# Performance work log

Measured on AMD Instinct MI355X. Metric: run time of the kernel, lower is better.

The kernel has to match this reference:

```python
import jax, jax.numpy as jnp
import numpy as np

B = 131072
D = 64          # d_model
T = 4           # num_tiles
TEMP = 0.5


def setup_inputs() -> dict:
    key = jax.random.key(0)
    ks = jax.random.split(key, 16)
    s = 0.02
    return {
        "a_vec": jax.random.normal(ks[0], (B, D), dtype=jnp.float32),
        "b_vec": jax.random.normal(ks[1], (B, D), dtype=jnp.float32),
        "pos_encoding": jax.random.normal(ks[2], (B, 8), dtype=jnp.float32),
        # router: Linear(2D+8 -> D), GELU, Linear(D -> T)
        "Wr1": jax.random.normal(ks[3], (2 * D + 8, D), dtype=jnp.float32) * s,
        "br1": jnp.zeros((D,), dtype=jnp.float32),
        "Wr2": jax.random.normal(ks[4], (D, T), dtype=jnp.float32) * s,
        "br2": jnp.zeros((T,), dtype=jnp.float32),
        # tile nets: per-tile Linear(2D -> 2D), GELU, Linear(2D -> D)
        "W1": jax.random.normal(ks[5], (T, 2 * D, 2 * D), dtype=jnp.float32) * s,
        "b1": jnp.zeros((T, 2 * D), dtype=jnp.float32),
        "W2": jax.random.normal(ks[6], (T, 2 * D, D), dtype=jnp.float32) * s,
        "b2": jnp.zeros((T, D), dtype=jnp.float32),
    }


def _router(x, Wr1, br1, Wr2, br2):
    h = jax.nn.gelu(x @ Wr1 + br1, approximate=False)  # torch nn.GELU is exact
    return (h @ Wr2 + br2) / TEMP


def reference(a_vec, b_vec, pos_encoding, Wr1, br1, Wr2, br2, W1, b1, W2, b2):
    pair = jnp.concatenate([a_vec, b_vec], axis=-1)            # (B, 2D)

    # Routing 1 uses pair; routing 2 uses flipped pair. Both expert passes
    # consume `pair` (faithful to the original code, which feeds pair both times).
    idx1 = jnp.argmax(_router(jnp.concatenate([pair, pos_encoding], -1),
                              Wr1, br1, Wr2, br2), axis=-1)    # (B,)
    pair_flip = jnp.concatenate([b_vec, a_vec], axis=-1)
    idx2 = jnp.argmax(_router(jnp.concatenate([pair_flip, pos_encoding], -1),
                              Wr1, br1, Wr2, br2), axis=-1)    # (B,)

    # Run all tiles on every sample (small T), then gather the routed output.
    h = jax.nn.gelu(jnp.einsum('bi,tij->btj', pair, W1) + b1, approximate=False)  # (B,T,2D)
    out_all = jnp.einsum('bth,thd->btd', h, W2) + b2                              # (B,T,D)

    out1 = jnp.take_along_axis(out_all, idx1[:, None, None], axis=1)[:, 0]
    out2 = jnp.take_along_axis(out_all, idx2[:, None, None], axis=1)[:, 0]
    return out1, out2
```

## Files before the change

kernel.cpp:

```cpp
#include <hip/hip_runtime.h>

#define B_N 131072

using bfrag_t = __attribute__((ext_vector_type(8))) short;
using acc_t   = __attribute__((ext_vector_type(4))) float;
using v4f     = __attribute__((ext_vector_type(4))) float;
using i32x4_t = __attribute__((ext_vector_type(4))) int;

__device__ __forceinline__ unsigned short f2bf(float f) {
  unsigned int u = __float_as_uint(f);
  u += 0x7FFFu + ((u >> 16) & 1u);
  return (unsigned short)(u >> 16);
}

__device__ __forceinline__ unsigned int pk2bf(float x, float y) {
  return (unsigned int)f2bf(x) | ((unsigned int)f2bf(y) << 16);
}

__device__ __forceinline__ void gload_lds16(const void* g, void* l) {
  __builtin_amdgcn_global_load_lds((const __attribute__((address_space(1))) void*)g,
                                   (__attribute__((address_space(3))) void*)l, 16, 0, 0);
}

__device__ __forceinline__ float gelu_f(float x) {
  float ax = fabsf(x) * 0.70710678118654752f;
  float t  = __builtin_amdgcn_rcpf(fmaf(0.3275911f, ax, 1.0f));
  float p  = fmaf(1.061405429f, t, -1.453152027f);
  p = fmaf(p, t, 1.421413741f);
  p = fmaf(p, t, -0.284496736f);
  p = fmaf(p, t, 0.254829592f);
  p = p * t;
  float e  = __expf(-ax * ax);
  float er = fmaf(-p, e, 1.0f);
  er = (x < 0.0f) ? -er : er;
  return 0.5f * x * (1.0f + er);
}

__global__ __launch_bounds__(256) void prepack2_k(
    const float* __restrict__ Wr1, const float* __restrict__ br1,
    const float* __restrict__ Wr2, const float* __restrict__ br2,
    const float* __restrict__ W1, const float* __restrict__ W2,
    float* __restrict__ RW, short* __restrict__ W1s, short* __restrict__ W2s) {
  int gt = blockIdx.x * 256 + threadIdx.x;
  for (int idx = gt; idx < 142 * 64; idx += 16384) {
    int row = idx >> 6, j = idx & 63; float val;
    if (row < 136)      val = Wr1[row * 64 + j];
    else if (row == 136) val = br1[j];
    else if (row < 141) val = Wr2[(row - 137) * 64 + j];
    else                val = (j < 4) ? br2[j] : 0.0f;
    RW[idx] = val;
  }
  for (int ch = gt; ch < 8192; ch += 16384) {
    int t = ch >> 11, r = (ch >> 4) & 127, c = ch & 15;
    const float* src = W1 + t * 16384 + r;
    short* dst = W1s + (t * 128 + r) * 128 + ((c ^ (r & 15)) * 8);
    #pragma unroll
    for (int m = 0; m < 8; m++) dst[m] = (short)f2bf(src[(c * 8 + m) * 128]);
  }
  for (int ch = gt; ch < 4096; ch += 16384) {
    int t = ch >> 10, d = (ch >> 4) & 63, c = ch & 15;
    const float* src = W2 + t * 8192 + d;
    short* dst = W2s + (t * 64 + d) * 128 + ((c ^ (d & 15)) * 8);
    #pragma unroll
    for (int m = 0; m < 8; m++) dst[m] = (short)f2bf(src[(c * 8 + m) * 64]);
  }
}

__global__ __launch_bounds__(256) void router4_k(
    const float* __restrict__ a, const float* __restrict__ b,
    const float* __restrict__ pos, const float* __restrict__ RW,
    unsigned char* __restrict__ r1, unsigned char* __restrict__ r2) {
  __shared__ float WB[142 * 64];
  int tid = threadIdx.x, wave = tid >> 6, lane = tid & 63;
  for (int it = 0; it < 9; it++) {
    int cb = it * 256 + wave * 64;
    if (cb < 2272) {
      int chunk = cb + lane;
      if (chunk < 2272) gload_lds16(RW + chunk * 4, (char*)WB + cb * 16);
    }
  }
  __syncthreads();
  int s = blockIdx.x * 256 + tid;
  v4f acc1[16], acc2[16];
  #pragma unroll
  for (int c = 0; c < 16; c++) {
    v4f binit = *(const v4f*)(WB + 136 * 64 + c * 4);
    acc1[c] = binit; acc2[c] = binit;
  }
  const acc_t* arow = (const acc_t*)(a + (size_t)s * 64);
  const acc_t* brow = (const acc_t*)(b + (size_t)s * 64);
  #pragma unroll 2
  for (int c4 = 0; c4 < 16; c4++) {
    acc_t av = arow[c4], bv = brow[c4];
    #pragma unroll
    for (int e = 0; e < 4; e++) {
      float x1 = av[e], x2 = bv[e];
      v4f x1v = {x1, x1, x1, x1}, x2v = {x2, x2, x2, x2};
      const v4f* w = (const v4f*)(WB + (c4 * 4 + e) * 64);
      #pragma unroll
      for (int c = 0; c < 16; c++) {
        acc1[c] = __builtin_elementwise_fma(x1v, w[c], acc1[c]);
        acc2[c] = __builtin_elementwise_fma(x2v, w[c], acc2[c]);
      }
    }
  }
  #pragma unroll 2
  for (int c4 = 0; c4 < 16; c4++) {
    acc_t av = arow[c4], bv = brow[c4];
    #pragma unroll
    for (int e = 0; e < 4; e++) {
      float x1 = bv[e], x2 = av[e];
      v4f x1v = {x1, x1, x1, x1}, x2v = {x2, x2, x2, x2};
      const v4f* w = (const v4f*)(WB + (64 + c4 * 4 + e) * 64);
      #pragma unroll
      for (int c = 0; c < 16; c++) {
        acc1[c] = __builtin_elementwise_fma(x1v, w[c], acc1[c]);
        acc2[c] = __builtin_elementwise_fma(x2v, w[c], acc2[c]);
      }
    }
  }
  {
    const acc_t* prow = (const acc_t*)(pos + (size_t)s * 8);
    #pragma unroll
    for (int h = 0; h < 2; h++) {
      acc_t pv = prow[h];
      #pragma unroll
      for (int e = 0; e < 4; e++) {
        float p = pv[e];
        v4f p4 = {p, p, p, p};
        const v4f* wp = (const v4f*)(WB + (128 + h * 4 + e) * 64);
        #pragma unroll
        for (int c = 0; c < 16; c++) {
          acc1[c] = __builtin_elementwise_fma(p4, wp[c], acc1[c]);
          acc2[c] = __builtin_elementwise_fma(p4, wp[c], acc2[c]);
        }
      }
    }
  }
  v4f l1 = *(const v4f*)(WB + 141 * 64);
  v4f l2 = l1;
  #pragma unroll
  for (int c = 0; c < 16; c++) {
    #pragma unroll
    for (int m = 0; m < 4; m++) {
      float h1 = gelu_f(acc1[c][m]), h2 = gelu_f(acc2[c][m]);
      v4f w2 = *(const v4f*)(WB + 137 * 64 + (c * 4 + m) * 4);
      v4f h1v = {h1, h1, h1, h1}, h2v = {h2, h2, h2, h2};
      l1 = __builtin_elementwise_fma(h1v, w2, l1);
      l2 = __builtin_elementwise_fma(h2v, w2, l2);
    }
  }
  int idx1 = 0; float b1v = l1[0];
  if (l1[1] > b1v) { b1v = l1[1]; idx1 = 1; }
  if (l1[2] > b1v) { b1v = l1[2]; idx1 = 2; }
  if (l1[3] > b1v) { b1v = l1[3]; idx1 = 3; }
  int idx2 = 0; float b2v = l2[0];
  if (l2[1] > b2v) { b2v = l2[1]; idx2 = 1; }
  if (l2[2] > b2v) { b2v = l2[2]; idx2 = 2; }
  if (l2[3] > b2v) { b2v = l2[3]; idx2 = 3; }
  r1[s] = (unsigned char)idx1;
  r2[s] = (unsigned char)idx2;
}

__global__ __launch_bounds__(256) void expert2_k(
    const float* __restrict__ a, const float* __restrict__ b,
    const short* __restrict__ W1s, const short* __restrict__ W2s,
    const float* __restrict__ b1, const float* __restrict__ b2,
    const unsigned char* __restrict__ r1, const unsigned char* __restrict__ r2,
    float* __restrict__ out) {
  __shared__ short LB[24576];
  int tid = threadIdx.x;
  int wave = tid >> 6, lane = tid & 63;
  int q = lane >> 4, sm = lane & 15;
  int s0 = blockIdx.x * 128;

  #pragma unroll
  for (int r = 0; r < 8; r++) {
    int slot = r * 256 + tid;
    int g = slot >> 10, sg = slot & 1023;
    int f = sg >> 6, l = sg & 63;
    int sgrp = f >> 2, kb = f & 3;
    int s = s0 + g * 64 + sgrp * 16 + (l & 15);
    int k = kb * 32 + (l >> 4) * 8;
    const float* src = (k < 64) ? (a + s * 64 + k) : (b + s * 64 + (k - 64));
    acc_t v0 = *(const acc_t*)(src);
    acc_t v1 = *(const acc_t*)(src + 4);
    i32x4_t pk;
    pk[0] = (int)pk2bf(v0[0], v0[1]);
    pk[1] = (int)pk2bf(v0[2], v0[3]);
    pk[2] = (int)pk2bf(v1[0], v1[1]);
    pk[3] = (int)pk2bf(v1[2], v1[3]);
    *(i32x4_t*)(&LB[slot * 8]) = pk;
  }
  __syncthreads();
  bfrag_t bfrag[2][4];
  #pragma unroll
  for (int g = 0; g < 2; g++)
    #pragma unroll
    for (int kb = 0; kb < 4; kb++)
      bfrag[g][kb] = *(const bfrag_t*)(&LB[((g * 16 + wave * 4 + kb) * 64 + lane) * 8]);

  int sA = s0 + wave * 16 + sm, sB = sA + 64;
  int i1A = (int)r1[sA], i2A = (int)r2[sA];
  int i1B = (int)r1[sB], i2B = (int)r2[sB];
  __syncthreads();

  acc_t zero = {0.f, 0.f, 0.f, 0.f};
  acc_t o1[2][4], o2[2][4];
  #pragma unroll
  for (int g = 0; g < 2; g++)
    #pragma unroll
    for (int i = 0; i < 4; i++) { o1[g][i] = zero; o2[g][i] = zero; }

  int vb[4];
  #pragma unroll
  for (int kb = 0; kb < 4; kb++) vb[kb] = sm * 256 + (((kb * 4 + q) ^ sm) * 16);
  int addr0 = (((q & 1) * 2) * 16 + sm) * 4;
  int addr1 = addr0 + 64;
  bool hi = (q >> 1) != 0;

  for (int t = 0; t < 4; t++) {
    #pragma unroll
    for (int it = 0; it < 12; it++) {
      int cb = it * 256 + wave * 64;
      int chunk = cb + lane;
      const short* gsrc = (chunk < 2048) ? (W1s + t * 16384 + chunk * 8)
                                         : (W2s + t * 8192 + (chunk - 2048) * 8);
      gload_lds16(gsrc, (char*)LB + cb * 16);
    }
    __syncthreads();
    #pragma unroll
    for (int g = 0; g < 2; g++) {
      unsigned int hp[8][2];
      #pragma unroll
      for (int mt = 0; mt < 8; mt++) {
        acc_t c = zero;
        #pragma unroll
        for (int kb = 0; kb < 4; kb++) {
          bfrag_t A = *(const bfrag_t*)((const char*)LB + mt * 4096 + vb[kb]);
          c = __builtin_amdgcn_mfma_f32_16x16x32_bf16(A, bfrag[g][kb], c, 0, 0, 0);
        }
        acc_t bv = *(const acc_t*)(b1 + t * 128 + mt * 16 + q * 4);
        float g0 = gelu_f(c[0] + bv[0]);
        float g1 = gelu_f(c[1] + bv[1]);
        float g2 = gelu_f(c[2] + bv[2]);
        float g3 = gelu_f(c[3] + bv[3]);
        hp[mt][0] = pk2bf(g0, g1);
        hp[mt][1] = pk2bf(g2, g3);
      }
      bfrag_t b2f[4];
      #pragma unroll
      for (int kb2 = 0; kb2 < 4; kb2++) {
        int p00 = __builtin_amdgcn_ds_bpermute(addr0, (int)hp[2 * kb2][0]);
        int p01 = __builtin_amdgcn_ds_bpermute(addr0, (int)hp[2 * kb2][1]);
        int p10 = __builtin_amdgcn_ds_bpermute(addr1, (int)hp[2 * kb2][0]);
        int p11 = __builtin_amdgcn_ds_bpermute(addr1, (int)hp[2 * kb2][1]);
        int q00 = __builtin_amdgcn_ds_bpermute(addr0, (int)hp[2 * kb2 + 1][0]);
        int q01 = __builtin_amdgcn_ds_bpermute(addr0, (int)hp[2 * kb2 + 1][1]);
        int q10 = __builtin_amdgcn_ds_bpermute(addr1, (int)hp[2 * kb2 + 1][0]);
        int q11 = __builtin_amdgcn_ds_bpermute(addr1, (int)hp[2 * kb2 + 1][1]);
        i32x4_t w;
        w[0] = hi ? q00 : p00;
        w[1] = hi ? q01 : p01;
        w[2] = hi ? q10 : p10;
        w[3] = hi ? q11 : p11;
        b2f[kb2] = __builtin_bit_cast(bfrag_t, w);
      }
      int i1g = g ? i1B : i1A;
      int i2g = g ? i2B : i2A;
      #pragma unroll
      for (int mt2 = 0; mt2 < 4; mt2++) {
        acc_t c = zero;
        #pragma unroll
        for (int kb2 = 0; kb2 < 4; kb2++) {
          bfrag_t A = *(const bfrag_t*)((const char*)LB + 32768 + mt2 * 4096 + vb[kb2]);
          c = __builtin_amdgcn_mfma_f32_16x16x32_bf16(A, b2f[kb2], c, 0, 0, 0);
        }
        acc_t bv = *(const acc_t*)(b2 + t * 64 + mt2 * 16 + q * 4);
        c[0] += bv[0]; c[1] += bv[1]; c[2] += bv[2]; c[3] += bv[3];
        o1[g][mt2] = (i1g == t) ? c : o1[g][mt2];
        o2[g][mt2] = (i2g == t) ? c : o2[g][mt2];
      }
    }
    __syncthreads();
  }
  #pragma unroll
  for (int g = 0; g < 2; g++) {
    int so = g ? sB : sA;
    float* p1 = out + so * 64 + q * 4;
    float* p2 = out + (size_t)B_N * 64 + so * 64 + q * 4;
    #pragma unroll
    for (int mt2 = 0; mt2 < 4; mt2++) {
      *(acc_t*)(p1 + mt2 * 16) = o1[g][mt2];
      *(acc_t*)(p2 + mt2 * 16) = o2[g][mt2];
    }
  }
}

extern "C" void kernel_launch(void* const* d_in, const int* in_sizes, int n_in,
                              void* d_out, int out_size, void* d_ws, size_t ws_size,
                              hipStream_t stream) {
  const float* a   = (const float*)d_in[0];
  const float* bv  = (const float*)d_in[1];
  const float* pos = (const float*)d_in[2];
  const float* Wr1 = (const float*)d_in[3];
  const float* br1 = (const float*)d_in[4];
  const float* Wr2 = (const float*)d_in[5];
  const float* br2 = (const float*)d_in[6];
  const float* W1  = (const float*)d_in[7];
  const float* b1  = (const float*)d_in[8];
  const float* W2  = (const float*)d_in[9];
  const float* b2  = (const float*)d_in[10];
  float* out = (float*)d_out;

  unsigned char* r1 = (unsigned char*)d_ws;
  unsigned char* r2 = r1 + B_N;
  float* RW  = (float*)((char*)d_ws + 262144);
  short* W1s = (short*)((char*)d_ws + 298496);
  short* W2s = (short*)((char*)d_ws + 429568);

  prepack2_k<<<64, 256, 0, stream>>>(Wr1, br1, Wr2, br2, W1, W2, RW, W1s, W2s);
  router4_k<<<B_N / 256, 256, 0, stream>>>(a, bv, pos, RW, r1, r2);
  expert2_k<<<B_N / 128, 256, 0, stream>>>(a, bv, W1s, W2s, b1, b2, r1, r2, out);
}
```

Before: 281.7 us.

## Split router across four threads per sample with LDS-staged transposed inputs

Rewrites the router kernel so each sample is handled by four threads, each computing a quarter of the hidden units, cutting per-thread accumulators from 128 to 32 floats. Inputs a, b and pos are loaded coalesced and stored transposed with padding into shared memory, and GELU outputs are exchanged through shared memory for the second layer. This targets register pressure, low occupancy and uncoalesced per-thread row loads, at the cost of more shared memory per block, extra barriers, and redundant second-layer work across the four threads.

```diff
diff --git a/kernel.cpp b/kernel.cpp
--- a/kernel.cpp
+++ b/kernel.cpp
@@ -66,89 +66,116 @@
   }
 }
 
-__global__ __launch_bounds__(256) void router4_k(
+__global__ __launch_bounds__(256) void router6_k(
     const float* __restrict__ a, const float* __restrict__ b,
     const float* __restrict__ pos, const float* __restrict__ RW,
     unsigned char* __restrict__ r1, unsigned char* __restrict__ r2) {
-  __shared__ float WB[142 * 64];
+  __shared__ float SB[17928];
+  const int XA = 9088, XB = 13248, PP = 17408;
   int tid = threadIdx.x, wave = tid >> 6, lane = tid & 63;
+  int s0 = blockIdx.x * 64;
+
   for (int it = 0; it < 9; it++) {
     int cb = it * 256 + wave * 64;
     if (cb < 2272) {
       int chunk = cb + lane;
-      if (chunk < 2272) gload_lds16(RW + chunk * 4, (char*)WB + cb * 16);
-    }
-  }
-  __syncthreads();
-  int s = blockIdx.x * 256 + tid;
-  v4f acc1[16], acc2[16];
-  #pragma unroll
-  for (int c = 0; c < 16; c++) {
-    v4f binit = *(const v4f*)(WB + 136 * 64 + c * 4);
-    acc1[c] = binit; acc2[c] = binit;
-  }
-  const acc_t* arow = (const acc_t*)(a + (size_t)s * 64);
-  const acc_t* brow = (const acc_t*)(b + (size_t)s * 64);
+      if (chunk < 2272) gload_lds16(RW + chunk * 4, (char*)SB + cb * 16);
+    }
+  }
+  #pragma unroll
+  for (int it = 0; it < 4; it++) {
+    int idx = it * 256 + tid;
+    int s = idx >> 4, c = idx & 15;
+    v4f va = *(const v4f*)(a + (size_t)(s0 + s) * 64 + c * 4);
+    v4f vb = *(const v4f*)(b + (size_t)(s0 + s) * 64 + c * 4);
+    #pragma unroll
+    for (int k = 0; k < 4; k++) {
+      SB[XA + (c * 4 + k) * 65 + s] = va[k];
+      SB[XB + (c * 4 + k) * 65 + s] = vb[k];
+    }
+  }
+  #pragma unroll
+  for (int r = 0; r < 2; r++) {
+    int idx = r * 256 + tid;
+    int s = idx >> 3, c = idx & 7;
+    SB[PP + c * 65 + s] = pos[(size_t)(s0 + s) * 8 + c];
+  }
+  __syncthreads();
+
+  int sq = tid >> 2, jq = tid & 3;
+  v4f acc1[4], acc2[4];
+  #pragma unroll
+  for (int e = 0; e < 4; e++) {
+    v4f bi = *(const v4f*)(SB + 136 * 64 + jq * 16 + e * 4);
+    acc1[e] = bi; acc2[e] = bi;
+  }
+  #pragma unroll 4
+  for (int i = 0; i < 64; ++i) {
+    float xa = SB[XA + i * 65 + sq];
+    float xb = SB[XB + i * 65 + sq];
+    const v4f* w = (const v4f*)(SB + i * 64 + jq * 16);
+    v4f xav = {xa, xa, xa, xa}, xbv = {xb, xb, xb, xb};
+    #pragma unroll
+    for (int e = 0; e < 4; e++) {
+      v4f wv = w[e];
+      acc1[e] = __builtin_elementwise_fma(xav, wv, acc1[e]);
+      acc2[e] = __builtin_elementwise_fma(xbv, wv, acc2[e]);
+    }
+  }
+  #pragma unroll 4
+  for (int i = 0; i < 64; ++i) {
+    float xa = SB[XA + i * 65 + sq];
+    float xb = SB[XB + i * 65 + sq];
+    const v4f* w = (const v4f*)(SB + (64 + i) * 64 + jq * 16);
+    v4f xav = {xa, xa, xa, xa}, xbv = {xb, xb, xb, xb};
+    #pragma unroll
+    for (int e = 0; e < 4; e++) {
+      v4f wv = w[e];
+      acc1[e] = __builtin_elementwise_fma(xbv, wv, acc1[e]);
+      acc2[e] = __builtin_elementwise_fma(xav, wv, acc2[e]);
+    }
+  }
   #pragma unroll 2
-  for (int c4 = 0; c4 < 16; c4++) {
-    acc_t av = arow[c4], bv = brow[c4];
+  for (int i = 0; i < 8; ++i) {
+    float p = SB[PP + i * 65 + sq];
+    const v4f* w = (const v4f*)(SB + (128 + i) * 64 + jq * 16);
+    v4f pv = {p, p, p, p};
     #pragma unroll
     for (int e = 0; e < 4; e++) {
-      float x1 = av[e], x2 = bv[e];
-      v4f x1v = {x1, x1, x1, x1}, x2v = {x2, x2, x2, x2};
-      const v4f* w = (const v4f*)(WB + (c4 * 4 + e) * 64);
-      #pragma unroll
-      for (int c = 0; c < 16; c++) {
-        acc1[c] = __builtin_elementwise_fma(x1v, w[c], acc1[c]);
-        acc2[c] = __builtin_elementwise_fma(x2v, w[c], acc2[c]);
-      }
-    }
-  }
-  #pragma unroll 2
-  for (int c4 = 0; c4 < 16; c4++) {
-    acc_t av = arow[c4], bv = brow[c4];
-    #pragma unroll
-    for (int e = 0; e < 4; e++) {
-      float x1 = bv[e], x2 = av[e];
-      v4f x1v = {x1, x1, x1, x1}, x2v = {x2, x2, x2, x2};
-      const v4f* w = (const v4f*)(WB + (64 + c4 * 4 + e) * 64);
-      #pragma unroll
-      for (int c = 0; c < 16; c++) {
-        acc1[c] = __builtin_elementwise_fma(x1v, w[c], acc1[c]);
-        acc2[c] = __builtin_elementwise_fma(x2v, w[c], acc2[c]);
-      }
-    }
-  }
-  {
-    const acc_t* prow = (const acc_t*)(pos + (size_t)s * 8);
-    #pragma unroll
-    for (int h = 0; h < 2; h++) {
-      acc_t pv = prow[h];
-      #pragma unroll
-      for (int e = 0; e < 4; e++) {
-        float p = pv[e];
-        v4f p4 = {p, p, p, p};
-        const v4f* wp = (const v4f*)(WB + (128 + h * 4 + e) * 64);
-        #pragma unroll
-        for (int c = 0; c < 16; c++) {
-          acc1[c] = __builtin_elementwise_fma(p4, wp[c], acc1[c]);
-          acc2[c] = __builtin_elementwise_fma(p4, wp[c], acc2[c]);
-        }
-      }
-    }
-  }
-  v4f l1 = *(const v4f*)(WB + 141 * 64);
+      v4f wv = w[e];
+      acc1[e] = __builtin_elementwise_fma(pv, wv, acc1[e]);
+      acc2[e] = __builtin_elementwise_fma(pv, wv, acc2[e]);
+    }
+  }
+  #pragma unroll
+  for (int e = 0; e < 4; e++) {
+    #pragma unroll
+    for (int c = 0; c < 4; c++) {
+      acc1[e][c] = gelu_f(acc1[e][c]);
+      acc2[e][c] = gelu_f(acc2[e][c]);
+    }
+  }
+  __syncthreads();
+  #pragma unroll
+  for (int e = 0; e < 4; e++) {
+    #pragma unroll
+    for (int c = 0; c < 4; c++) {
+      int j = jq * 16 + e * 4 + c;
+      SB[XA + j * 65 + sq] = acc1[e][c];
+      SB[XB + j * 65 + sq] = acc2[e][c];
+    }
+  }
+  __syncthreads();
+  v4f l1 = *(const v4f*)(SB + 141 * 64);
   v4f l2 = l1;
-  #pragma unroll
-  for (int c = 0; c < 16; c++) {
-    #pragma unroll
-    for (int m = 0; m < 4; m++) {
-      float h1 = gelu_f(acc1[c][m]), h2 = gelu_f(acc2[c][m]);
-      v4f w2 = *(const v4f*)(WB + 137 * 64 + (c * 4 + m) * 4);
-      v4f h1v = {h1, h1, h1, h1}, h2v = {h2, h2, h2, h2};
-      l1 = __builtin_elementwise_fma(h1v, w2, l1);
-      l2 = __builtin_elementwise_fma(h2v, w2, l2);
-    }
+  #pragma unroll 4
+  for (int j = 0; j < 64; ++j) {
+    float h1 = SB[XA + j * 65 + sq];
+    float h2 = SB[XB + j * 65 + sq];
+    v4f w2 = *(const v4f*)(SB + 137 * 64 + j * 4);
+    v4f h1v = {h1, h1, h1, h1}, h2v = {h2, h2, h2, h2};
+    l1 = __builtin_elementwise_fma(h1v, w2, l1);
+    l2 = __builtin_elementwise_fma(h2v, w2, l2);
   }
   int idx1 = 0; float b1v = l1[0];
   if (l1[1] > b1v) { b1v = l1[1]; idx1 = 1; }
@@ -158,8 +185,10 @@
   if (l2[1] > b2v) { b2v = l2[1]; idx2 = 1; }
   if (l2[2] > b2v) { b2v = l2[2]; idx2 = 2; }
   if (l2[3] > b2v) { b2v = l2[3]; idx2 = 3; }
-  r1[s] = (unsigned char)idx1;
-  r2[s] = (unsigned char)idx2;
+  if (jq == 0) {
+    r1[s0 + sq] = (unsigned char)idx1;
+    r2[s0 + sq] = (unsigned char)idx2;
+  }
 }
 
 __global__ __launch_bounds__(256) void expert2_k(
@@ -320,6 +349,6 @@
   short* W2s = (short*)((char*)d_ws + 429568);
 
   prepack2_k<<<64, 256, 0, stream>>>(Wr1, br1, Wr2, br2, W1, W2, RW, W1s, W2s);
-  router4_k<<<B_N / 256, 256, 0, stream>>>(a, bv, pos, RW, r1, r2);
+  router6_k<<<B_N / 64, 256, 0, stream>>>(a, bv, pos, RW, r1, r2);
   expert2_k<<<B_N / 128, 256, 0, stream>>>(a, bv, W1s, W2s, b1, b2, r1, r2, out);
 }
```

Measured after the change: 271.6 us. 1.04x faster.
